# Performance work log

Measured on AMD Instinct MI355X. Metric: run time of the kernel, lower is better.

Reference implementation:

```python
import jax, jax.numpy as jnp
import numpy as np

MIN_PERSISTENCE = [0.0, 0.0]  # from init kwargs, one per homology dimension


def setup_inputs() -> dict:
    key = jax.random.key(0)
    k1, k2, k3 = jax.random.split(key, 3)
    D = 512
    N = D * D * D  # 134,217,728 voxels
    P = 2_000_000  # persistence pairs per homology dimension
    X = jax.random.normal(k1, (D, D, D), dtype=jnp.float32)
    # Stand-ins for GUDHI cofaces_of_persistence_pairs() output:
    # flat (birth_idx, death_idx) pairs into Xflat, interleaved, per dimension.
    indices0 = jax.random.randint(k2, (2 * P,), 0, N, dtype=jnp.int32)
    indices1 = jax.random.randint(k3, (2 * P,), 0, N, dtype=jnp.int32)
    return {"X": X, "indices0": indices0, "indices1": indices1}


def _diagram(Xflat, indices, min_pers):
    # gather birth/death filtration values -> [num_pairs, 2]
    dgm = jnp.take(Xflat, indices).reshape(-1, 2)
    if min_pers >= 0:
        # Original uses tf.where + gather (dynamic shape). For jit we keep a
        # fixed shape and zero out points with persistence <= min_pers.
        keep = jnp.abs(dgm[:, 1] - dgm[:, 0]) > min_pers
        dgm = jnp.where(keep[:, None], dgm, jnp.zeros((), dgm.dtype))
    return dgm


def reference(X, indices0, indices1):
    Xflat = X.reshape(-1)
    dgm0 = _diagram(Xflat, indices0, MIN_PERSISTENCE[0])
    dgm1 = _diagram(Xflat, indices1, MIN_PERSISTENCE[1])
    return (dgm0, dgm1)
```

## Files before the change

kernel.cpp:

```cpp
#include <hip/hip_runtime.h>
#include <hip/hip_bf16.h>


typedef int   v4i __attribute__((ext_vector_type(4)));
typedef float v4f __attribute__((ext_vector_type(4)));

__global__ __launch_bounds__(256) void gather_diagram_kernel(
    const float* __restrict__ X,
    const int* __restrict__ idx0,
    const int* __restrict__ idx1,
    float* __restrict__ out,
    int n4_0,
    int n4_total)
{
    constexpr int C = 4;
    const int tid    = blockIdx.x * blockDim.x + threadIdx.x;
    const int stride = gridDim.x * blockDim.x;

    int  c[C];
    v4i  ij[C];
    bool ok[C];
    #pragma unroll
    for (int j = 0; j < C; ++j) {
        c[j]  = tid + j * stride;
        ok[j] = c[j] < n4_total;
        int cc = ok[j] ? c[j] : 0;
        const v4i* p = (cc < n4_0)
            ? reinterpret_cast<const v4i*>(idx0) + cc
            : reinterpret_cast<const v4i*>(idx1) + (cc - n4_0);
        ij[j] = __builtin_nontemporal_load(p);
    }

    float v[C][4];
    #pragma unroll
    for (int j = 0; j < C; ++j) {
        v[j][0] = X[ij[j].x];
        v[j][1] = X[ij[j].y];
        v[j][2] = X[ij[j].z];
        v[j][3] = X[ij[j].w];
    }

    #pragma unroll
    for (int j = 0; j < C; ++j) {
        bool k0 = v[j][1] != v[j][0];
        bool k1 = v[j][3] != v[j][2];
        v4f o;
        o.x = k0 ? v[j][0] : 0.0f;
        o.y = k0 ? v[j][1] : 0.0f;
        o.z = k1 ? v[j][2] : 0.0f;
        o.w = k1 ? v[j][3] : 0.0f;
        if (ok[j])
            __builtin_nontemporal_store(o, reinterpret_cast<v4f*>(out) + c[j]);
    }
}

extern "C" void kernel_launch(void* const* d_in, const int* in_sizes, int n_in,
                              void* d_out, int out_size, void* d_ws, size_t ws_size,
                              hipStream_t stream) {
    const float* X        = (const float*)d_in[0];
    const int*   indices0 = (const int*)d_in[1];
    const int*   indices1 = (const int*)d_in[2];
    float*       out      = (float*)d_out;

    const int n4_0     = in_sizes[1] / 4;
    const int n4_total = (in_sizes[1] + in_sizes[2]) / 4;

    constexpr int C = 4, BLOCK = 256;
    const int threads_needed = (n4_total + C - 1) / C;
    const int blocks = (threads_needed + BLOCK - 1) / BLOCK;

    gather_diagram_kernel<<<blocks, BLOCK, 0, stream>>>(
        X, indices0, indices1, out, n4_0, n4_total);
}
```

Baseline: 750.8 us.

## Bucket gather indices by address range before gathering to improve locality

```diff
diff --git a/kernel.cpp b/kernel.cpp
--- a/kernel.cpp
+++ b/kernel.cpp
@@ -1,17 +1,106 @@
 #include <hip/hip_runtime.h>
-#include <hip/hip_bf16.h>
 
 
 typedef int   v4i __attribute__((ext_vector_type(4)));
+typedef int   v2i __attribute__((ext_vector_type(2)));
 typedef float v4f __attribute__((ext_vector_type(4)));
+
+#define NBINS     2048
+#define BIN_SHIFT 16
+#define BIN_CAP   8192
+
+__global__ void zero_counts_kernel(int* __restrict__ counts) {
+    int t = blockIdx.x * blockDim.x + threadIdx.x;
+    if (t < NBINS) counts[t] = 0;
+}
+
+__global__ __launch_bounds__(256) void partition_kernel(
+    const int* __restrict__ idx0, const int* __restrict__ idx1,
+    int* __restrict__ counts, v2i* __restrict__ entries,
+    int n4_0, int n4_total, int ch4)
+{
+    __shared__ int lhist[NBINS];
+    const int t  = threadIdx.x;
+    const int c0 = blockIdx.x * ch4;
+    const int c1 = min(c0 + ch4, n4_total);
+
+    for (int i = t; i < NBINS; i += 256) lhist[i] = 0;
+    __syncthreads();
+
+    for (int c = c0 + t; c < c1; c += 256) {
+        const v4i* p = (c < n4_0)
+            ? (reinterpret_cast<const v4i*>(idx0) + c)
+            : (reinterpret_cast<const v4i*>(idx1) + (c - n4_0));
+        v4i v = __builtin_nontemporal_load(p);
+        atomicAdd(&lhist[(((unsigned)v.x) >> BIN_SHIFT) & (NBINS - 1)], 1);
+        atomicAdd(&lhist[(((unsigned)v.y) >> BIN_SHIFT) & (NBINS - 1)], 1);
+        atomicAdd(&lhist[(((unsigned)v.z) >> BIN_SHIFT) & (NBINS - 1)], 1);
+        atomicAdd(&lhist[(((unsigned)v.w) >> BIN_SHIFT) & (NBINS - 1)], 1);
+    }
+    __syncthreads();
+
+    for (int b = t; b < NBINS; b += 256) {
+        int c = lhist[b];
+        lhist[b] = (c > 0) ? (b * BIN_CAP + atomicAdd(&counts[b], c)) : 0;
+    }
+    __syncthreads();
+
+    for (int c = c0 + t; c < c1; c += 256) {
+        const v4i* p = (c < n4_0)
+            ? (reinterpret_cast<const v4i*>(idx0) + c)
+            : (reinterpret_cast<const v4i*>(idx1) + (c - n4_0));
+        v4i v = __builtin_nontemporal_load(p);
+        const int pos = c * 4;
+        #pragma unroll
+        for (int k = 0; k < 4; ++k) {
+            int id = (k == 0) ? v.x : (k == 1) ? v.y : (k == 2) ? v.z : v.w;
+            int b  = (((unsigned)id) >> BIN_SHIFT) & (NBINS - 1);
+            int slot = atomicAdd(&lhist[b], 1);
+            if (slot >= b * BIN_CAP && slot < (b + 1) * BIN_CAP) {
+                v2i e; e.x = id; e.y = pos + k;
+                entries[slot] = e;
+            }
+        }
+    }
+}
+
+__global__ __launch_bounds__(256) void gather_bins_kernel(
+    const float* __restrict__ X, const int* __restrict__ counts,
+    const v2i* __restrict__ entries, float* __restrict__ out)
+{
+    const int b = blockIdx.x;
+    int cnt = counts[b];
+    if (cnt > BIN_CAP) cnt = BIN_CAP;
+    const v2i* e = entries + (size_t)b * BIN_CAP;
+    for (int i = threadIdx.x; i < cnt; i += 256) {
+        v2i p = e[i];
+        out[p.y] = X[p.x];
+    }
+}
+
+__global__ __launch_bounds__(256) void pair_filter_kernel(
+    float* __restrict__ out, int n4)
+{
+    int i = blockIdx.x * 256 + threadIdx.x;
+    if (i >= n4) return;
+    v4f* p = reinterpret_cast<v4f*>(out) + i;
+    v4f o = *p;
+    bool k0 = o.y != o.x;
+    bool k1 = o.w != o.z;
+    v4f r;
+    r.x = k0 ? o.x : 0.0f;
+    r.y = k0 ? o.y : 0.0f;
+    r.z = k1 ? o.z : 0.0f;
+    r.w = k1 ? o.w : 0.0f;
+    *p = r;
+}
 
 __global__ __launch_bounds__(256) void gather_diagram_kernel(
     const float* __restrict__ X,
     const int* __restrict__ idx0,
     const int* __restrict__ idx1,
     float* __restrict__ out,
-    int n4_0,
-    int n4_total)
+    int n4_0, int n4_total)
 {
     constexpr int C = 4;
     const int tid    = blockIdx.x * blockDim.x + threadIdx.x;
@@ -62,13 +151,35 @@
     const int*   indices1 = (const int*)d_in[2];
     float*       out      = (float*)d_out;
 
-    const int n4_0     = in_sizes[1] / 4;
-    const int n4_total = (in_sizes[1] + in_sizes[2]) / 4;
+    const int n0       = in_sizes[1];
+    const int n1       = in_sizes[2];
+    const int n4_0     = n0 / 4;
+    const int n4_total = (n0 + n1) / 4;
 
-    constexpr int C = 4, BLOCK = 256;
-    const int threads_needed = (n4_total + C - 1) / C;
-    const int blocks = (threads_needed + BLOCK - 1) / BLOCK;
+    const size_t entries_off = 65536;
+    const size_t ws_need = entries_off + (size_t)NBINS * BIN_CAP * sizeof(int) * 2;
 
-    gather_diagram_kernel<<<blocks, BLOCK, 0, stream>>>(
-        X, indices0, indices1, out, n4_0, n4_total);
+    if (ws_size < ws_need || (n0 & 3) || (n1 & 3) || n4_total <= 0 || d_ws == nullptr) {
+        constexpr int C = 4, BLOCK = 256;
+        const int threads_needed = (n4_total + C - 1) / C;
+        const int blocks = (threads_needed + BLOCK - 1) / BLOCK;
+        if (blocks > 0)
+            gather_diagram_kernel<<<blocks, BLOCK, 0, stream>>>(
+                X, indices0, indices1, out, n4_0, n4_total);
+        return;
+    }
+
+    int* counts  = (int*)d_ws;
+    v2i* entries = (v2i*)((char*)d_ws + entries_off);
+
+    zero_counts_kernel<<<(NBINS + 255) / 256, 256, 0, stream>>>(counts);
+
+    constexpr int PART_BLOCKS = 256;
+    const int ch4 = (n4_total + PART_BLOCKS - 1) / PART_BLOCKS;
+    partition_kernel<<<PART_BLOCKS, 256, 0, stream>>>(
+        indices0, indices1, counts, entries, n4_0, n4_total, ch4);
+
+    gather_bins_kernel<<<NBINS, 256, 0, stream>>>(X, counts, entries, out);
+
+    pair_filter_kernel<<<(n4_total + 255) / 256, 256, 0, stream>>>(out, n4_total);
 }
```

Result: slower. 1.003 ms (+33.6%).

## Split gather into cache-sized X chunks with warm-up passes and separate filter

Applied to the files above, without the earlier changes.

```diff
diff --git a/kernel.cpp b/kernel.cpp
--- a/kernel.cpp
+++ b/kernel.cpp
@@ -1,17 +1,29 @@
 #include <hip/hip_runtime.h>
-#include <hip/hip_bf16.h>
 
 
 typedef int   v4i __attribute__((ext_vector_type(4)));
 typedef float v4f __attribute__((ext_vector_type(4)));
 
-__global__ __launch_bounds__(256) void gather_diagram_kernel(
+#define NCHUNK 8
+
+__global__ __launch_bounds__(256) void warm_kernel(
+    const v4f* __restrict__ Xc, int n16)
+{
+    int i = blockIdx.x * blockDim.x + threadIdx.x;
+    float acc = 0.0f;
+    if (i < n16) {
+        v4f v = Xc[i];
+        acc = v.x + v.y + v.z + v.w;
+    }
+    asm volatile("" :: "v"(acc));
+}
+
+__global__ __launch_bounds__(256) void gather_range_kernel(
     const float* __restrict__ X,
     const int* __restrict__ idx0,
     const int* __restrict__ idx1,
     float* __restrict__ out,
-    int n4_0,
-    int n4_total)
+    int n4_0, int n4_total, int lo, int hi)
 {
     constexpr int C = 4;
     const int tid    = blockIdx.x * blockDim.x + threadIdx.x;
@@ -28,7 +40,63 @@
         const v4i* p = (cc < n4_0)
             ? reinterpret_cast<const v4i*>(idx0) + cc
             : reinterpret_cast<const v4i*>(idx1) + (cc - n4_0);
-        ij[j] = __builtin_nontemporal_load(p);
+        ij[j] = *p;
+    }
+
+    #pragma unroll
+    for (int j = 0; j < C; ++j) {
+        if (!ok[j]) continue;
+        float* o = out + 4 * (size_t)c[j];
+        #pragma unroll
+        for (int k = 0; k < 4; ++k) {
+            int id = (k == 0) ? ij[j].x : (k == 1) ? ij[j].y
+                   : (k == 2) ? ij[j].z : ij[j].w;
+            if (id >= lo && id < hi)
+                o[k] = X[id];
+        }
+    }
+}
+
+__global__ __launch_bounds__(256) void pair_filter_kernel(
+    float* __restrict__ out, int n4)
+{
+    int i = blockIdx.x * 256 + threadIdx.x;
+    if (i >= n4) return;
+    v4f* p = reinterpret_cast<v4f*>(out) + i;
+    v4f o = *p;
+    bool k0 = o.y != o.x;
+    bool k1 = o.w != o.z;
+    v4f r;
+    r.x = k0 ? o.x : 0.0f;
+    r.y = k0 ? o.y : 0.0f;
+    r.z = k1 ? o.z : 0.0f;
+    r.w = k1 ? o.w : 0.0f;
+    *p = r;
+}
+
+__global__ __launch_bounds__(256) void gather_diagram_kernel(
+    const float* __restrict__ X,
+    const int* __restrict__ idx0,
+    const int* __restrict__ idx1,
+    float* __restrict__ out,
+    int n4_0, int n4_total)
+{
+    constexpr int C = 4;
+    const int tid    = blockIdx.x * blockDim.x + threadIdx.x;
+    const int stride = gridDim.x * blockDim.x;
+
+    int  c[C];
+    v4i  ij[C];
+    bool ok[C];
+    #pragma unroll
+    for (int j = 0; j < C; ++j) {
+        c[j]  = tid + j * stride;
+        ok[j] = c[j] < n4_total;
+        int cc = ok[j] ? c[j] : 0;
+        const v4i* p = (cc < n4_0)
+            ? reinterpret_cast<const v4i*>(idx0) + cc
+            : reinterpret_cast<const v4i*>(idx1) + (cc - n4_0);
+        ij[j] = *p;
     }
 
     float v[C][4];
@@ -49,8 +117,10 @@
         o.y = k0 ? v[j][1] : 0.0f;
         o.z = k1 ? v[j][2] : 0.0f;
         o.w = k1 ? v[j][3] : 0.0f;
-        if (ok[j])
-            __builtin_nontemporal_store(o, reinterpret_cast<v4f*>(out) + c[j]);
+        if (ok[j]) {
+            v4f* po = reinterpret_cast<v4f*>(out) + c[j];
+            *po = o;
+        }
     }
 }
 
@@ -62,13 +132,38 @@
     const int*   indices1 = (const int*)d_in[2];
     float*       out      = (float*)d_out;
 
-    const int n4_0     = in_sizes[1] / 4;
-    const int n4_total = (in_sizes[1] + in_sizes[2]) / 4;
+    const int nX       = in_sizes[0];
+    const int n0       = in_sizes[1];
+    const int n1       = in_sizes[2];
+    const int n4_0     = n0 / 4;
+    const int n4_total = (n0 + n1) / 4;
+
+    if ((n0 & 3) || (n1 & 3) || n4_total <= 0 || nX <= 0) {
+        constexpr int C = 4, BLOCK = 256;
+        const int threads_needed = (n4_total + C - 1) / C;
+        const int blocks = (threads_needed + BLOCK - 1) / BLOCK;
+        if (blocks > 0)
+            gather_diagram_kernel<<<blocks, BLOCK, 0, stream>>>(
+                X, indices0, indices1, out, n4_0, n4_total);
+        return;
+    }
 
     constexpr int C = 4, BLOCK = 256;
     const int threads_needed = (n4_total + C - 1) / C;
-    const int blocks = (threads_needed + BLOCK - 1) / BLOCK;
+    const int gblocks = (threads_needed + BLOCK - 1) / BLOCK;
 
-    gather_diagram_kernel<<<blocks, BLOCK, 0, stream>>>(
-        X, indices0, indices1, out, n4_0, n4_total);
+    const int chunk = (nX + NCHUNK - 1) / NCHUNK;
+    for (int p = 0; p < NCHUNK; ++p) {
+        const int lo = p * chunk;
+        if (lo >= nX) break;
+        const int hi = (lo + chunk < nX) ? (lo + chunk) : nX;
+        const int n16 = (hi - lo) / 4;
+        if (n16 > 0)
+            warm_kernel<<<(n16 + BLOCK - 1) / BLOCK, BLOCK, 0, stream>>>(
+                reinterpret_cast<const v4f*>(X + lo), n16);
+        gather_range_kernel<<<gblocks, BLOCK, 0, stream>>>(
+            X, indices0, indices1, out, n4_0, n4_total, lo, hi);
+    }
+
+    pair_filter_kernel<<<(n4_total + 255) / 256, 256, 0, stream>>>(out, n4_total);
 }
```

Result: slower. 932.5 us (+24.2%).
